# Kernel optimization log

Measured on AMD Instinct MI355X. Metric: run time of the kernel, lower is better.

## Reference

```python
import jax, jax.numpy as jnp
import numpy as np

BATCH = 1024
SEQ = 512
HID = 512
OUT = 10


def setup_inputs() -> dict:
    key = jax.random.key(0)
    k1, k2, k3, k4 = jax.random.split(key, 4)
    # Xavier-ish scaled params (scale irrelevant for correctness baseline)
    x = jax.random.normal(k1, (BATCH, SEQ), dtype=jnp.float32)
    W_hx = jax.random.normal(k2, (HID, 1), dtype=jnp.float32) * (1.0 / np.sqrt(1 + HID)).astype(np.float32)
    W_hh = jax.random.normal(k3, (HID, HID), dtype=jnp.float32) * (1.0 / np.sqrt(2 * HID)).astype(np.float32)
    W_yh = jax.random.normal(k4, (OUT, HID), dtype=jnp.float32) * (1.0 / np.sqrt(HID + OUT)).astype(np.float32)
    b_h = jnp.zeros((HID, 1), dtype=jnp.float32)
    b_y = jnp.zeros((OUT, 1), dtype=jnp.float32)
    return {"x": x, "W_hx": W_hx, "W_hh": W_hh, "W_yh": W_yh, "b_h": b_h, "b_y": b_y}


def reference(x, W_hx, W_hh, W_yh, b_h, b_y):
    # x: [B, T]; hidden state h: [H, B] (column-major layout as in the torch code)
    B = x.shape[0]
    H = W_hh.shape[0]
    xs = x.T  # [T, B], scan over time

    def step(h, x_t):
        # x_t: [B] -> treated as [1, B]; W_hx: [H, 1]
        h_new = jnp.tanh(W_hx @ x_t[None, :] + W_hh @ h + b_h)  # [H, B]
        return h_new, None

    h0 = jnp.zeros((H, B), dtype=x.dtype)
    h_T, _ = jax.lax.scan(step, h0, xs)
    y = W_yh @ h_T + b_y  # [O, B] — only the last timestep's output is returned
    return y.T  # [B, O]
```

## Files before the change

kernel.cpp:

```cpp
#include <hip/hip_runtime.h>


#define BATCH 1024
#define SEQT  512
#define HID   512
#define OUTD  10
#define KR    12
#define NKK   16

typedef _Float16 f16;
typedef _Float16 f16x8 __attribute__((ext_vector_type(8)));
typedef _Float16 f16x4 __attribute__((ext_vector_type(4)));
typedef float    f32x4 __attribute__((ext_vector_type(4)));

__global__ void wconv_kernel(const float* __restrict__ Whh, f16* __restrict__ frag) {
    int id = blockIdx.x * blockDim.x + threadIdx.x;
    int lane = id & 63;
    int kk   = (id >> 6) & 15;
    int mt   = (id >> 10) & 3;
    int g    = id >> 12;
    int m = g * 64 + mt * 16 + (lane & 15);
    int k = kk * 32 + ((lane >> 4) & 3) * 8;
    const float* src = Whh + (size_t)m * HID + k;
    f16x8 v;
#pragma unroll
    for (int j = 0; j < 8; ++j) v[j] = (f16)src[j];
    *(f16x8*)(frag + (size_t)id * 8) = v;
}

__device__ __forceinline__ float fast_tanh(float v) {
    v = fminf(fmaxf(v, -15.f), 15.f);
    float e = __expf(2.f * v);
    return (e - 1.f) * __builtin_amdgcn_rcpf(e + 1.f);
}

__global__ __launch_bounds__(512)
__attribute__((amdgpu_waves_per_eu(2, 2)))
void rnn_cu(
    const f16* __restrict__ frag,
    f16* __restrict__ hG,
    const float* __restrict__ x,
    const float* __restrict__ Whx,
    const float* __restrict__ bh)
{
    __shared__ f16 HB[8192];
    __shared__ f16 WL[65536];

    const int tid  = threadIdx.x;
    const int w    = tid >> 6;
    const int lane = tid & 63;
    const int n    = lane & 15;
    const int q    = lane >> 4;
    const int bg   = blockIdx.x;

    {
        f16x8 z;
#pragma unroll
        for (int j = 0; j < 8; ++j) z[j] = (f16)0.f;
        *(f16x8*)&HB[tid * 16]     = z;
        *(f16x8*)&HB[tid * 16 + 8] = z;
    }

    const f16x8* A = (const f16x8*)frag;

#pragma unroll
    for (int mt = 0; mt < 4; ++mt)
#pragma unroll
        for (int kkl = 0; kkl < 4; ++kkl) {
            int e = ((w * 4 + mt) * 4 + kkl) * 64 + lane;
            *(f16x8*)&WL[e * 8] = A[((w * 4 + mt) * 16 + (KR + kkl)) * 64 + lane];
        }

    f16x8 Wr[KR * 4];
#pragma unroll
    for (int kk = 0; kk < KR; ++kk)
#pragma unroll
        for (int mt = 0; mt < 4; ++mt)
            Wr[kk * 4 + mt] = A[((w * 4 + mt) * 16 + kk) * 64 + lane];

    __syncthreads();

    const int b = bg * 16 + n;
    const float* xp = x + (size_t)b * SEQT;

#pragma unroll 1
    for (int s = 0; s < SEQT; ++s) {
        float xv = xp[s];

        f32x4 acc[4] = {{0,0,0,0},{0,0,0,0},{0,0,0,0},{0,0,0,0}};

#pragma unroll
        for (int kk = 0; kk < KR; ++kk) {
            f16x8 bf = *(const f16x8*)&HB[(kk * 64 + lane) * 8];
#pragma unroll
            for (int mt = 0; mt < 4; ++mt)
                acc[mt] = __builtin_amdgcn_mfma_f32_16x16x32_f16(
                    Wr[kk * 4 + mt], bf, acc[mt], 0, 0, 0);
        }
#pragma unroll
        for (int kkl = 0; kkl < 4; ++kkl) {
            f16x8 bf = *(const f16x8*)&HB[((KR + kkl) * 64 + lane) * 8];
#pragma unroll
            for (int mt = 0; mt < 4; ++mt) {
                f16x8 a = *(const f16x8*)&WL[(((w * 4 + mt) * 4 + kkl) * 64 + lane) * 8];
                acc[mt] = __builtin_amdgcn_mfma_f32_16x16x32_f16(
                    a, bf, acc[mt], 0, 0, 0);
            }
        }

        __syncthreads();

        const float* wbp = Whx;
        const float* bbp = bh;
        asm volatile("" : "+v"(wbp), "+v"(bbp));

#pragma unroll
        for (int mt = 0; mt < 4; ++mt) {
            int m0 = w * 64 + mt * 16 + q * 4;
            f32x4 whx4 = *(const f32x4*)(wbp + m0);
            f32x4 bh4  = *(const f32x4*)(bbp + m0);
            f16x4 hv;
#pragma unroll
            for (int r = 0; r < 4; ++r) {
                float pre = acc[mt][r] + whx4[r] * xv + bh4[r];
                hv[r] = (f16)fast_tanh(pre);
            }
            int kkd = w * 2 + (mt >> 1);
            int q2  = (mt & 1) * 2 + (q >> 1);
            int j0  = (q & 1) * 4;
            int off = (kkd * 64 + q2 * 16 + n) * 8 + j0;
            if (s < SEQT - 1) {
                *(f16x4*)&HB[off] = hv;
            } else {
                *(f16x4*)(hG + (size_t)(((bg * 16 + kkd) * 64 + q2 * 16 + n) * 8 + j0)) = hv;
            }
        }

        __syncthreads();
    }
}

__global__ __launch_bounds__(256) void y_kernel(
    const f16* __restrict__ h, const float* __restrict__ Wyh,
    const float* __restrict__ by, float* __restrict__ out)
{
    int id = blockIdx.x * blockDim.x + threadIdx.x;
    if (id >= BATCH * OUTD) return;
    int b = id / OUTD, o = id % OUTD;
    int bg = b >> 4, n = b & 15;
    const float* wrow = Wyh + (size_t)o * HID;
    float s = by[o];
    for (int kk = 0; kk < 16; ++kk)
#pragma unroll
        for (int q2 = 0; q2 < 4; ++q2) {
            f16x8 hv = *(const f16x8*)(h + (size_t)((bg * 16 + kk) * 64 + q2 * 16 + n) * 8);
            const float* wp = wrow + kk * 32 + q2 * 8;
#pragma unroll
            for (int j = 0; j < 8; ++j) s += wp[j] * (float)hv[j];
        }
    out[id] = s;
}

extern "C" void kernel_launch(void* const* d_in, const int* in_sizes, int n_in,
                              void* d_out, int out_size, void* d_ws, size_t ws_size,
                              hipStream_t stream) {
    const float* x   = (const float*)d_in[0];
    const float* Whx = (const float*)d_in[1];
    const float* Whh = (const float*)d_in[2];
    const float* Wyh = (const float*)d_in[3];
    const float* bh  = (const float*)d_in[4];
    const float* by  = (const float*)d_in[5];
    float* out = (float*)d_out;

    char* ws   = (char*)d_ws;
    f16*  hG   = (f16*)ws;
    f16*  frag = (f16*)(ws + (2 << 20));

    wconv_kernel<<<128, 256, 0, stream>>>(Whh, frag);
    rnn_cu<<<64, 512, 0, stream>>>(frag, hG, x, Whx, bh);
    y_kernel<<<(BATCH * OUTD + 255) / 256, 256, 0, stream>>>(hG, Wyh, by, out);
}
```

Before: 1.309 ms.

## Double-buffer hidden state, drop mid-step barrier, stream tail weights from global

After: 1.754 ms. 34.0% more time.

```diff
diff --git a/kernel.cpp b/kernel.cpp
--- a/kernel.cpp
+++ b/kernel.cpp
@@ -43,8 +43,7 @@
     const float* __restrict__ Whx,
     const float* __restrict__ bh)
 {
-    __shared__ f16 HB[8192];
-    __shared__ f16 WL[65536];
+    __shared__ f16 HB[2][8192];
 
     const int tid  = threadIdx.x;
     const int w    = tid >> 6;
@@ -53,23 +52,17 @@
     const int q    = lane >> 4;
     const int bg   = blockIdx.x;
 
+    f16* hb0 = &HB[0][0];
+
     {
         f16x8 z;
 #pragma unroll
         for (int j = 0; j < 8; ++j) z[j] = (f16)0.f;
-        *(f16x8*)&HB[tid * 16]     = z;
-        *(f16x8*)&HB[tid * 16 + 8] = z;
+        *(f16x8*)&hb0[tid * 16]     = z;
+        *(f16x8*)&hb0[tid * 16 + 8] = z;
     }
 
     const f16x8* A = (const f16x8*)frag;
-
-#pragma unroll
-    for (int mt = 0; mt < 4; ++mt)
-#pragma unroll
-        for (int kkl = 0; kkl < 4; ++kkl) {
-            int e = ((w * 4 + mt) * 4 + kkl) * 64 + lane;
-            *(f16x8*)&WL[e * 8] = A[((w * 4 + mt) * 16 + (KR + kkl)) * 64 + lane];
-        }
 
     f16x8 Wr[KR * 4];
 #pragma unroll
@@ -78,6 +71,8 @@
         for (int mt = 0; mt < 4; ++mt)
             Wr[kk * 4 + mt] = A[((w * 4 + mt) * 16 + kk) * 64 + lane];
 
+    const f16x8* Aw = A + ((size_t)(w * 4) * 16 + KR) * 64 + lane;
+
     __syncthreads();
 
     const int b = bg * 16 + n;
@@ -85,13 +80,30 @@
 
 #pragma unroll 1
     for (int s = 0; s < SEQT; ++s) {
+        const f16* hbr = hb0 + ((s & 1) << 13);
+        f16*       hbw = hb0 + (((s & 1) ^ 1) << 13);
+
+        const float* wbp = Whx;
+        const float* bbp = bh;
+        const f16x8* Awp = Aw;
+        asm volatile("" : "+v"(wbp), "+v"(bbp), "+v"(Awp));
+
         float xv = xp[s];
+        f32x4 av[4];
+#pragma unroll
+        for (int mt = 0; mt < 4; ++mt) {
+            int m0 = w * 64 + mt * 16 + q * 4;
+            f32x4 w4 = *(const f32x4*)(wbp + m0);
+            f32x4 b4 = *(const f32x4*)(bbp + m0);
+#pragma unroll
+            for (int r = 0; r < 4; ++r) av[mt][r] = b4[r] + w4[r] * xv;
+        }
 
         f32x4 acc[4] = {{0,0,0,0},{0,0,0,0},{0,0,0,0},{0,0,0,0}};
 
 #pragma unroll
         for (int kk = 0; kk < KR; ++kk) {
-            f16x8 bf = *(const f16x8*)&HB[(kk * 64 + lane) * 8];
+            f16x8 bf = *(const f16x8*)&hbr[(kk * 64 + lane) * 8];
 #pragma unroll
             for (int mt = 0; mt < 4; ++mt)
                 acc[mt] = __builtin_amdgcn_mfma_f32_16x16x32_f16(
@@ -99,38 +111,27 @@
         }
 #pragma unroll
         for (int kkl = 0; kkl < 4; ++kkl) {
-            f16x8 bf = *(const f16x8*)&HB[((KR + kkl) * 64 + lane) * 8];
+            f16x8 bf = *(const f16x8*)&hbr[((KR + kkl) * 64 + lane) * 8];
 #pragma unroll
             for (int mt = 0; mt < 4; ++mt) {
-                f16x8 a = *(const f16x8*)&WL[(((w * 4 + mt) * 4 + kkl) * 64 + lane) * 8];
+                f16x8 a = Awp[((size_t)mt * 16 + kkl) * 64];
                 acc[mt] = __builtin_amdgcn_mfma_f32_16x16x32_f16(
                     a, bf, acc[mt], 0, 0, 0);
             }
         }
 
-        __syncthreads();
-
-        const float* wbp = Whx;
-        const float* bbp = bh;
-        asm volatile("" : "+v"(wbp), "+v"(bbp));
-
 #pragma unroll
         for (int mt = 0; mt < 4; ++mt) {
-            int m0 = w * 64 + mt * 16 + q * 4;
-            f32x4 whx4 = *(const f32x4*)(wbp + m0);
-            f32x4 bh4  = *(const f32x4*)(bbp + m0);
             f16x4 hv;
 #pragma unroll
-            for (int r = 0; r < 4; ++r) {
-                float pre = acc[mt][r] + whx4[r] * xv + bh4[r];
-                hv[r] = (f16)fast_tanh(pre);
-            }
+            for (int r = 0; r < 4; ++r)
+                hv[r] = (f16)fast_tanh(acc[mt][r] + av[mt][r]);
             int kkd = w * 2 + (mt >> 1);
             int q2  = (mt & 1) * 2 + (q >> 1);
             int j0  = (q & 1) * 4;
             int off = (kkd * 64 + q2 * 16 + n) * 8 + j0;
             if (s < SEQT - 1) {
-                *(f16x4*)&HB[off] = hv;
+                *(f16x4*)&hbw[off] = hv;
             } else {
                 *(f16x4*)(hG + (size_t)(((bg * 16 + kkd) * 64 + q2 * 16 + n) * 8 + j0)) = hv;
             }
```

## Rebalance register/LDS split of W_hh and prefetch LDS operands in RNN loop

Applied to the files above, without the earlier changes.

Measured after the change: 1.469 ms. 1.12x slower.

```diff
diff --git a/kernel.cpp b/kernel.cpp
--- a/kernel.cpp
+++ b/kernel.cpp
@@ -5,8 +5,6 @@
 #define SEQT  512
 #define HID   512
 #define OUTD  10
-#define KR    12
-#define NKK   16
 
 typedef _Float16 f16;
 typedef _Float16 f16x8 __attribute__((ext_vector_type(8)));
@@ -28,6 +26,16 @@
     *(f16x8*)(frag + (size_t)id * 8) = v;
 }
 
+__global__ void prep_kernel(const float* __restrict__ Whx,
+                            const float* __restrict__ bh,
+                            f16* __restrict__ wxbh) {
+    int m = blockIdx.x * blockDim.x + threadIdx.x;
+    if (m < HID) {
+        wxbh[2 * m]     = (f16)Whx[m];
+        wxbh[2 * m + 1] = (f16)bh[m];
+    }
+}
+
 __device__ __forceinline__ float fast_tanh(float v) {
     v = fminf(fmaxf(v, -15.f), 15.f);
     float e = __expf(2.f * v);
@@ -40,11 +48,10 @@
     const f16* __restrict__ frag,
     f16* __restrict__ hG,
     const float* __restrict__ x,
-    const float* __restrict__ Whx,
-    const float* __restrict__ bh)
+    const f16* __restrict__ wxbh)
 {
     __shared__ f16 HB[8192];
-    __shared__ f16 WL[65536];
+    __shared__ f16 WL[73728];
 
     const int tid  = threadIdx.x;
     const int w    = tid >> 6;
@@ -64,65 +71,91 @@
     const f16x8* A = (const f16x8*)frag;
 
 #pragma unroll
-    for (int mt = 0; mt < 4; ++mt)
-#pragma unroll
-        for (int kkl = 0; kkl < 4; ++kkl) {
-            int e = ((w * 4 + mt) * 4 + kkl) * 64 + lane;
-            *(f16x8*)&WL[e * 8] = A[((w * 4 + mt) * 16 + (KR + kkl)) * 64 + lane];
-        }
-
-    f16x8 Wr[KR * 4];
-#pragma unroll
-    for (int kk = 0; kk < KR; ++kk)
+    for (int f = 0; f < 18; ++f) {
+        int kk = (f < 2) ? 11 : 12 + ((f - 2) >> 2);
+        int mt = (f < 2) ? 2 + f : ((f - 2) & 3);
+        *(f16x8*)&WL[((w * 18 + f) * 64 + lane) * 8] =
+            A[((w * 4 + mt) * 16 + kk) * 64 + lane];
+    }
+
+    f16x8 Wr[46];
+#pragma unroll
+    for (int kk = 0; kk < 11; ++kk)
 #pragma unroll
         for (int mt = 0; mt < 4; ++mt)
             Wr[kk * 4 + mt] = A[((w * 4 + mt) * 16 + kk) * 64 + lane];
+    Wr[44] = A[((w * 4 + 0) * 16 + 11) * 64 + lane];
+    Wr[45] = A[((w * 4 + 1) * 16 + 11) * 64 + lane];
 
     __syncthreads();
 
-    const int b = bg * 16 + n;
-    const float* xp = x + (size_t)b * SEQT;
+    const float* xp = x + (size_t)(bg * 16 + n) * SEQT;
 
 #pragma unroll 1
     for (int s = 0; s < SEQT; ++s) {
         float xv = xp[s];
 
+        const f16* wlb = &WL[(size_t)w * 18 * 64 * 8];
+        asm volatile("" : "+v"(wlb));
+
         f32x4 acc[4] = {{0,0,0,0},{0,0,0,0},{0,0,0,0},{0,0,0,0}};
 
-#pragma unroll
-        for (int kk = 0; kk < KR; ++kk) {
-            f16x8 bf = *(const f16x8*)&HB[(kk * 64 + lane) * 8];
-#pragma unroll
-            for (int mt = 0; mt < 4; ++mt)
-                acc[mt] = __builtin_amdgcn_mfma_f32_16x16x32_f16(
-                    Wr[kk * 4 + mt], bf, acc[mt], 0, 0, 0);
+        f16x8 hb[3];
+#pragma unroll
+        for (int i = 0; i < 3; ++i)
+            hb[i] = *(const f16x8*)&HB[(i * 64 + lane) * 8];
+
+        f16x8 wA0, wA1;
+        f16x8 wg[4];
+
+#pragma unroll
+        for (int kk = 0; kk < 16; ++kk) {
+            f16x8 bf = hb[kk % 3];
+            if (kk + 3 < 16)
+                hb[kk % 3] = *(const f16x8*)&HB[((kk + 3) * 64 + lane) * 8];
+
+            if (kk < 11) {
+#pragma unroll
+                for (int mt = 0; mt < 4; ++mt)
+                    acc[mt] = __builtin_amdgcn_mfma_f32_16x16x32_f16(
+                        Wr[kk * 4 + mt], bf, acc[mt], 0, 0, 0);
+            } else if (kk == 11) {
+                acc[0] = __builtin_amdgcn_mfma_f32_16x16x32_f16(Wr[44], bf, acc[0], 0, 0, 0);
+                acc[1] = __builtin_amdgcn_mfma_f32_16x16x32_f16(Wr[45], bf, acc[1], 0, 0, 0);
+                acc[2] = __builtin_amdgcn_mfma_f32_16x16x32_f16(wA0,    bf, acc[2], 0, 0, 0);
+                acc[3] = __builtin_amdgcn_mfma_f32_16x16x32_f16(wA1,    bf, acc[3], 0, 0, 0);
+            } else {
+#pragma unroll
+                for (int mt = 0; mt < 4; ++mt)
+                    acc[mt] = __builtin_amdgcn_mfma_f32_16x16x32_f16(
+                        wg[mt], bf, acc[mt], 0, 0, 0);
+            }
+
+            if (kk == 10) {
+                wA0 = *(const f16x8*)&wlb[(0 * 64 + lane) * 8];
+                wA1 = *(const f16x8*)&wlb[(1 * 64 + lane) * 8];
+#pragma unroll
+                for (int j = 0; j < 4; ++j)
+                    wg[j] = *(const f16x8*)&wlb[((2 + j) * 64 + lane) * 8];
+            } else if (kk >= 12 && kk < 15) {
+                const int fb = 2 + (kk - 11) * 4;
+#pragma unroll
+                for (int j = 0; j < 4; ++j)
+                    wg[j] = *(const f16x8*)&wlb[((fb + j) * 64 + lane) * 8];
+            }
         }
-#pragma unroll
-        for (int kkl = 0; kkl < 4; ++kkl) {
-            f16x8 bf = *(const f16x8*)&HB[((KR + kkl) * 64 + lane) * 8];
-#pragma unroll
-            for (int mt = 0; mt < 4; ++mt) {
-                f16x8 a = *(const f16x8*)&WL[(((w * 4 + mt) * 4 + kkl) * 64 + lane) * 8];
-                acc[mt] = __builtin_amdgcn_mfma_f32_16x16x32_f16(
-                    a, bf, acc[mt], 0, 0, 0);
-            }
-        }
 
         __syncthreads();
 
-        const float* wbp = Whx;
-        const float* bbp = bh;
-        asm volatile("" : "+v"(wbp), "+v"(bbp));
-
+        const f16* wp = wxbh;
+        asm volatile("" : "+v"(wp));
 #pragma unroll
         for (int mt = 0; mt < 4; ++mt) {
-            int m0 = w * 64 + mt * 16 + q * 4;
-            f32x4 whx4 = *(const f32x4*)(wbp + m0);
-            f32x4 bh4  = *(const f32x4*)(bbp + m0);
+            f16x8 wb = *(const f16x8*)(wp + (size_t)(w * 64 + mt * 16 + q * 4) * 2);
             f16x4 hv;
 #pragma unroll
             for (int r = 0; r < 4; ++r) {
-                float pre = acc[mt][r] + whx4[r] * xv + bh4[r];
+                float pre = fmaf((float)wb[2 * r], xv, acc[mt][r]) + (float)wb[2 * r + 1];
                 hv[r] = (f16)fast_tanh(pre);
             }
             int kkd = w * 2 + (mt >> 1);
@@ -174,9 +207,11 @@
 
     char* ws   = (char*)d_ws;
     f16*  hG   = (f16*)ws;
-    f16*  frag = (f16*)(ws + (2 << 20));
+    f16*  frag = (f16*)(ws + (1 << 20));
+    f16*  wxbh = (f16*)(ws + (3 << 19));
 
     wconv_kernel<<<128, 256, 0, stream>>>(Whh, frag);
-    rnn_cu<<<64, 512, 0, stream>>>(frag, hG, x, Whx, bh);
+    prep_kernel<<<2, 256, 0, stream>>>(Whx, bh, wxbh);
+    rnn_cu<<<64, 512, 0, stream>>>(frag, hG, x, wxbh);
     y_kernel<<<(BATCH * OUTD + 255) / 256, 256, 0, stream>>>(hG, Wyh, by, out);
 }
```
